# Kernel tuning notes

Measured on AMD Instinct MI355X. Metric: run time of the kernel, lower is better.

## Reference

```python
import jax, jax.numpy as jnp
import numpy as np

N_NODES = 100000
N_EDGES = 50000
NNZ = 1600000
D_IN = 128
D_OUT = 128  # heads(8) * out_channels(16)


def setup_inputs() -> dict:
    key = jax.random.key(0)
    k1, k2, k3, k4 = jax.random.split(key, 4)
    X = jax.random.normal(k1, (N_NODES, D_IN), dtype=jnp.float32)
    W = jax.random.normal(k2, (D_IN, D_OUT), dtype=jnp.float32) * (1.0 / np.sqrt(D_IN))
    eps = jnp.zeros((1,), dtype=jnp.float32)
    vertex = jax.random.randint(k3, (NNZ,), 0, N_NODES, dtype=jnp.int32)
    edges = jax.random.randint(k4, (NNZ,), 0, N_EDGES, dtype=jnp.int32)
    return {"X": X, "W": W, "eps": eps, "vertex": vertex, "edges": edges,
            "num_edges": N_EDGES}


def reference(X, W, eps, vertex, edges, num_edges):
    N = X.shape[0]
    Xp = X @ W                                   # [N, D_OUT] linear proj (no bias)
    Xve = Xp[vertex]                             # [nnz, D_OUT] vertex -> incidence gather
    Xe = jax.ops.segment_sum(Xve, edges, num_segments=num_edges)   # [E, D_OUT] first_aggregate='sum'
    Xev = Xe[edges]                              # [nnz, D_OUT] edge -> incidence gather
    Xv = jax.ops.segment_sum(Xev, vertex, num_segments=N)          # [N, D_OUT]
    out = (1.0 + eps) * Xp + Xv                  # GIN combine with learnable eps (eps is [1], broadcasts)
    return jax.nn.gelu(out, approximate=False)   # torch F.gelu default = exact erf
```

## Files before the change

kernel.cpp:

```cpp
#include <hip/hip_runtime.h>
#include <math.h>

#define NN 100000
#define NE 50000
#define NSEG (NE + NN)
#define DD 128

#define NBE 196
#define NBV 391
#define NB  (NBE + NBV)
#define CAP_E 8960
#define CAP_V 4608

typedef short bf16x8 __attribute__((ext_vector_type(8)));
typedef float f32x4 __attribute__((ext_vector_type(4)));
typedef float v2f __attribute__((ext_vector_type(2)));

static __device__ __forceinline__ float gelu_exact(float x) {
  return 0.5f * x * (1.0f + erff(x * 0.70710678118654752f));
}

static __device__ __forceinline__ int bucket_base(int g) {
  return (g < NBE) ? g * CAP_E : NBE * CAP_E + (g - NBE) * CAP_V;
}

static __device__ __forceinline__ void acc2(v2f& a, unsigned u) {
  union { unsigned i; float f; } lo, hi;
  lo.i = u << 16;
  hi.i = u & 0xFFFF0000u;
  v2f t;
  t.x = lo.f;
  t.y = hi.f;
  a += t;
}

static __device__ __forceinline__ void acc4(v2f* a, uint4 u) {
  acc2(a[0], u.x); acc2(a[1], u.y); acc2(a[2], u.z); acc2(a[3], u.w);
}

static __device__ __forceinline__ unsigned pack_bf16x2(float a, float b) {
  unsigned ua = __float_as_uint(a), ub = __float_as_uint(b);
  ua = (ua + 0x7FFFu + ((ua >> 16) & 1u)) >> 16;
  ub = (ub + 0x7FFFu + ((ub >> 16) & 1u)) >> 16;
  return ua | (ub << 16);
}

static __device__ __forceinline__ unsigned short bf16_rne(float a) {
  unsigned ua = __float_as_uint(a);
  ua = (ua + 0x7FFFu + ((ua >> 16) & 1u)) >> 16;
  return (unsigned short)ua;
}

static __device__ __forceinline__ void reduce8(v2f* a) {
#pragma unroll
  for (int k = 0; k < 4; ++k) {
    float x = a[k].x, y = a[k].y;
    x += __shfl_xor(x, 8);  y += __shfl_xor(y, 8);
    x += __shfl_xor(x, 16); y += __shfl_xor(y, 16);
    x += __shfl_xor(x, 32); y += __shfl_xor(y, 32);
    a[k].x = x; a[k].y = y;
  }
}

__global__ __launch_bounds__(256) void k_init(int* __restrict__ gcur,
                                              const float* __restrict__ W,
                                              unsigned short* __restrict__ Wt) {
  const int b = blockIdx.x;
  if (b < 64) {
    int idx = b * 256 + threadIdx.x;
    int k = idx >> 7, n = idx & 127;
    Wt[n * 128 + k] = bf16_rne(W[idx]);
  } else {
    int g = (b - 64) * 256 + threadIdx.x;
    if (g < NB) gcur[g] = bucket_base(g);
  }
}

__global__ __launch_bounds__(256) void k_gemm(const float* __restrict__ X,
                                              const unsigned short* __restrict__ Wt,
                                              unsigned short* __restrict__ Xb2h) {
  const int tid = threadIdx.x;
  const int w = tid >> 6;
  const int l = tid & 63;
  const int lm = l & 15;
  const int lk = l >> 4;
  const int R = blockIdx.x * 64 + w * 16;
  const int arow = R + lm;
  const bool rowok = arow < NN;
  const f32x4* __restrict__ X4 = (const f32x4*)X;
  const uint4* __restrict__ Wt4 = (const uint4*)Wt;

  f32x4 acc[8];
#pragma unroll
  for (int t = 0; t < 8; ++t) acc[t] = (f32x4)(0.f);

  for (int c = 0; c < 4; ++c) {
    const int k0 = c * 32 + lk * 8;
    f32x4 x0 = (f32x4)(0.f), x1 = (f32x4)(0.f);
    if (rowok) {
      x0 = __builtin_nontemporal_load(&X4[arow * 32 + (k0 >> 2)]);
      x1 = __builtin_nontemporal_load(&X4[arow * 32 + (k0 >> 2) + 1]);
    }
    union { bf16x8 v; uint4 u; } a;
    a.u.x = pack_bf16x2(x0.x, x0.y);
    a.u.y = pack_bf16x2(x0.z, x0.w);
    a.u.z = pack_bf16x2(x1.x, x1.y);
    a.u.w = pack_bf16x2(x1.z, x1.w);
#pragma unroll
    for (int t = 0; t < 8; ++t) {
      union { bf16x8 v; uint4 u; } b;
      b.u = Wt4[(t * 16 + lm) * 16 + c * 4 + lk];
      acc[t] = __builtin_amdgcn_mfma_f32_16x16x32_bf16(a.v, b.v, acc[t], 0, 0, 0);
    }
  }

  const int drow = R + lk * 4;
#pragma unroll
  for (int r = 0; r < 4; ++r) {
    const int row = drow + r;
    if (row < NN) {
#pragma unroll
      for (int t = 0; t < 8; ++t) {
        __builtin_nontemporal_store(
            bf16_rne(acc[t][r]),
            &Xb2h[((size_t)(t >> 2) * NN + row) * 64 + (t & 3) * 16 + lm]);
      }
    }
  }
}

__global__ __launch_bounds__(256) void k_pass1(const int* __restrict__ vertex,
                                               const int* __restrict__ edges,
                                               int* __restrict__ gcur,
                                               int* __restrict__ S, int nnz) {
  __shared__ int hist[NB];
  const int tid = threadIdx.x;
  for (int b = tid; b < NB; b += 256) hist[b] = 0;
  __syncthreads();
  const int base = blockIdx.x * 4096;
#pragma unroll
  for (int k = 0; k < 16; ++k) {
    int i = base + tid + k * 256;
    if (i < nnz) {
      atomicAdd(&hist[edges[i] >> 8], 1);
      atomicAdd(&hist[NBE + (vertex[i] >> 8)], 1);
    }
  }
  __syncthreads();
  for (int b = tid; b < NB; b += 256) {
    int c = hist[b];
    hist[b] = c ? atomicAdd(&gcur[b], c) : 0;
  }
  __syncthreads();
#pragma unroll
  for (int k = 0; k < 16; ++k) {
    int i = base + tid + k * 256;
    if (i < nnz) {
      int e = edges[i], v = vertex[i];
      int pe = atomicAdd(&hist[e >> 8], 1);
      S[pe] = ((e & 255) << 17) | v;
      int pv = atomicAdd(&hist[NBE + (v >> 8)], 1);
      S[pv] = ((v & 255) << 17) | e;
    }
  }
}

__global__ __launch_bounds__(256) void k_pass2(const int* __restrict__ gcur,
                                               const int* __restrict__ S,
                                               int* __restrict__ LE,
                                               unsigned short* __restrict__ LV,
                                               int* __restrict__ O, int nnz) {
  __shared__ int offs[257];
  __shared__ int cur[256];
  __shared__ int scratch[CAP_E];
  const int g = blockIdx.x;
  const int tid = threadIdx.x;
  int part = 0;
  for (int i = tid; i < g; i += 256) part += gcur[i] - bucket_base(i);
  cur[tid] = part;
  __syncthreads();
#pragma unroll
  for (int s2 = 128; s2 > 0; s2 >>= 1) {
    if (tid < s2) cur[tid] += cur[tid + s2];
    __syncthreads();
  }
  const bool isE = g < NBE;
  const int dbase = isE ? cur[0] : cur[0] - nnz;
  __syncthreads();

  const int sstart = bucket_base(g);
  int nit = gcur[g] - sstart;
  const int cap = isE ? CAP_E : CAP_V;
  if (nit > cap) nit = cap;
  const int s0 = isE ? (g << 8) : ((g - NBE) << 8);
  const int segN = min(256, (isE ? NE : NN) - s0);
  const int obase = isE ? s0 : NE + 1 + s0;
  for (int k = tid; k < 257; k += 256) offs[k] = 0;
  __syncthreads();
  for (int t = tid; t < nit; t += 256) atomicAdd(&offs[(S[sstart + t] >> 17) + 1], 1);
  __syncthreads();
  for (int off = 1; off < 256; off <<= 1) {
    int y = (tid >= off) ? offs[tid + 1 - off] : 0;
    __syncthreads();
    offs[tid + 1] += y;
    __syncthreads();
  }
  cur[tid] = offs[tid];
  __syncthreads();
  for (int t = tid; t < nit; t += 256) {
    int u = S[sstart + t];
    int r = atomicAdd(&cur[u >> 17], 1);
    scratch[r] = u & 0x1FFFF;
  }
  __syncthreads();
  if (isE) {
    for (int t = tid; t < nit; t += 256) LE[dbase + t] = scratch[t];
  } else {
    for (int t = tid; t < nit; t += 256) LV[dbase + t] = (unsigned short)scratch[t];
  }
  for (int k = tid; k <= segN; k += 256) O[obase + k] = dbase + offs[k];
}

__global__ __launch_bounds__(256) void k_edge_agg(const unsigned* __restrict__ Xb2h,
                                                  const int* __restrict__ O,
                                                  const int* __restrict__ LE,
                                                  unsigned* __restrict__ Xe2h) {
  const int h = blockIdx.y;
  const int e = blockIdx.x * 4 + (threadIdx.x >> 6);
  const int lane = threadIdx.x & 63;
  const int s = lane >> 3;
  const int r = lane & 7;
  const int start = O[e];
  const int end = O[e + 1];
  const uint4* __restrict__ P = (const uint4*)(Xb2h + (size_t)h * NN * 32);
  v2f a[4];
#pragma unroll
  for (int k = 0; k < 4; ++k) a[k] = (v2f)(0.f);
  int j = start + s;
  for (; j + 24 < end; j += 32) {
    int i0 = __builtin_nontemporal_load(&LE[j]);
    int i1 = __builtin_nontemporal_load(&LE[j + 8]);
    int i2 = __builtin_nontemporal_load(&LE[j + 16]);
    int i3 = __builtin_nontemporal_load(&LE[j + 24]);
    uint4 u0 = P[(size_t)i0 * 8 + r];
    uint4 u1 = P[(size_t)i1 * 8 + r];
    uint4 u2 = P[(size_t)i2 * 8 + r];
    uint4 u3 = P[(size_t)i3 * 8 + r];
    acc4(a, u0); acc4(a, u1); acc4(a, u2); acc4(a, u3);
  }
  if (j + 8 < end) {
    int i0 = __builtin_nontemporal_load(&LE[j]);
    int i1 = __builtin_nontemporal_load(&LE[j + 8]);
    uint4 u0 = P[(size_t)i0 * 8 + r];
    uint4 u1 = P[(size_t)i1 * 8 + r];
    acc4(a, u0); acc4(a, u1);
    j += 16;
  }
  if (j < end) {
    int i0 = __builtin_nontemporal_load(&LE[j]);
    acc4(a, P[(size_t)i0 * 8 + r]);
  }
  reduce8(a);
  const int p = s & 3;
  v2f sel = (p == 0) ? a[0] : (p == 1) ? a[1] : (p == 2) ? a[2] : a[3];
  unsigned pk = pack_bf16x2(sel.x, sel.y);
  if (s < 4) {
    __builtin_nontemporal_store(pk, &Xe2h[((size_t)h * NE + e) * 32 + r * 4 + p]);
  }
}

__global__ __launch_bounds__(256) void k_vert_agg(const unsigned* __restrict__ Xe2h,
                                                  const int* __restrict__ O,
                                                  const unsigned short* __restrict__ LV,
                                                  const float* __restrict__ eps,
                                                  const unsigned* __restrict__ Xb2h,
                                                  float* __restrict__ out) {
  const int h = blockIdx.y;
  const int v = blockIdx.x * 4 + (threadIdx.x >> 6);
  const int lane = threadIdx.x & 63;
  const int s = lane >> 3;
  const int r = lane & 7;
  const int start = O[NE + 1 + v];
  const int end = O[NE + 2 + v];
  const uint4* __restrict__ Q = (const uint4*)(Xe2h + (size_t)h * NE * 32);
  v2f a[4];
#pragma unroll
  for (int k = 0; k < 4; ++k) a[k] = (v2f)(0.f);
  int j = start + s;
  for (; j + 8 < end; j += 16) {
    int i0 = (int)__builtin_nontemporal_load(&LV[j]);
    int i1 = (int)__builtin_nontemporal_load(&LV[j + 8]);
    uint4 u0 = Q[(size_t)i0 * 8 + r];
    uint4 u1 = Q[(size_t)i1 * 8 + r];
    acc4(a, u0); acc4(a, u1);
  }
  if (j < end) {
    int i0 = (int)__builtin_nontemporal_load(&LV[j]);
    acc4(a, Q[(size_t)i0 * 8 + r]);
  }
  reduce8(a);
  const int p = s & 3;
  v2f sel = (p == 0) ? a[0] : (p == 1) ? a[1] : (p == 2) ? a[2] : a[3];
  unsigned su = __builtin_nontemporal_load(&Xb2h[((size_t)h * NN + v) * 32 + r * 4 + p]);
  union { unsigned i; float f; } plo, phi;
  plo.i = su << 16;
  phi.i = su & 0xFFFF0000u;
  const float sc = 1.0f + eps[0];
  v2f x;
  x.x = gelu_exact(fmaf(sc, plo.f, sel.x));
  x.y = gelu_exact(fmaf(sc, phi.f, sel.y));
  if (s < 4) {
    v2f* __restrict__ P2 = (v2f*)out;
    __builtin_nontemporal_store(x, &P2[(size_t)v * 64 + h * 32 + r * 4 + p]);
  }
}

extern "C" void kernel_launch(void* const* d_in, const int* in_sizes, int n_in,
                              void* d_out, int out_size, void* d_ws, size_t ws_size,
                              hipStream_t stream) {
  const float* X = (const float*)d_in[0];
  const float* W = (const float*)d_in[1];
  const float* eps = (const float*)d_in[2];
  const int* vertex = (const int*)d_in[3];
  const int* edges = (const int*)d_in[4];
  const int nnz = in_sizes[3];

  char* ws = (char*)d_ws;
  size_t off = 0;
  auto alloc = [&](size_t bytes) -> void* {
    void* p = ws + off;
    off = (off + bytes + 255) & ~(size_t)255;
    return p;
  };
  const size_t stagingB = ((size_t)NBE * CAP_E + (size_t)NBV * CAP_V) * 4;
  const size_t xbB = (size_t)NN * DD * 2;
  void* A = alloc(xbB > stagingB ? xbB : stagingB);
  int* S = (int*)A;
  unsigned short* Xb2h = (unsigned short*)A;
  unsigned* Xe2h = (unsigned*)alloc((size_t)NE * DD * 2);
  int* LE = (int*)alloc((size_t)nnz * sizeof(int));
  unsigned short* LV =
      (unsigned short*)alloc((size_t)nnz * sizeof(unsigned short));
  int* O = (int*)alloc((size_t)(NSEG + 2) * sizeof(int));
  int* gcur = (int*)alloc((size_t)NB * sizeof(int));
  unsigned short* Wt = (unsigned short*)alloc((size_t)DD * DD * 2);
  if (off > ws_size) return;

  k_init<<<67, 256, 0, stream>>>(gcur, W, Wt);
  k_pass1<<<(nnz + 4095) / 4096, 256, 0, stream>>>(vertex, edges, gcur, S, nnz);
  k_pass2<<<NB, 256, 0, stream>>>(gcur, S, LE, LV, O, nnz);
  k_gemm<<<(NN + 63) / 64, 256, 0, stream>>>(X, Wt, Xb2h);
  k_edge_agg<<<dim3(NE / 4, 2), 256, 0, stream>>>((const unsigned*)Xb2h, O, LE, Xe2h);
  k_vert_agg<<<dim3(NN / 4, 2), 256, 0, stream>>>(Xe2h, O, LV, eps,
                                                  (const unsigned*)Xb2h, (float*)d_out);
}
```

Baseline: 347.6 us.

## Drop head-split layout and gather full 256-byte rows per segment

Changes the bf16 projected and edge-feature buffers from a two-half, head-split layout to contiguous 128-wide rows. Each aggregation kernel now covers all 128 channels per segment in one pass, with 16 lanes per row and 4 rows in flight per wavefront. This halves the grid, reads each segment's index list once instead of twice, and shortens the cross-lane reduction. The trade is fewer independent rows per wave for short segments, and the GEMM stores lose their nontemporal hint.

```diff
diff --git a/kernel.cpp b/kernel.cpp
--- a/kernel.cpp
+++ b/kernel.cpp
@@ -51,11 +51,10 @@
   return (unsigned short)ua;
 }
 
-static __device__ __forceinline__ void reduce8(v2f* a) {
+static __device__ __forceinline__ void reduce4(v2f* a) {
 #pragma unroll
   for (int k = 0; k < 4; ++k) {
     float x = a[k].x, y = a[k].y;
-    x += __shfl_xor(x, 8);  y += __shfl_xor(y, 8);
     x += __shfl_xor(x, 16); y += __shfl_xor(y, 16);
     x += __shfl_xor(x, 32); y += __shfl_xor(y, 32);
     a[k].x = x; a[k].y = y;
@@ -78,7 +77,7 @@
 
 __global__ __launch_bounds__(256) void k_gemm(const float* __restrict__ X,
                                               const unsigned short* __restrict__ Wt,
-                                              unsigned short* __restrict__ Xb2h) {
+                                              unsigned short* __restrict__ Xb2) {
   const int tid = threadIdx.x;
   const int w = tid >> 6;
   const int l = tid & 63;
@@ -121,9 +120,7 @@
     if (row < NN) {
 #pragma unroll
       for (int t = 0; t < 8; ++t) {
-        __builtin_nontemporal_store(
-            bf16_rne(acc[t][r]),
-            &Xb2h[((size_t)(t >> 2) * NN + row) * 64 + (t & 3) * 16 + lm]);
+        Xb2[row * 128 + t * 16 + lm] = bf16_rne(acc[t][r]);
       }
     }
   }
@@ -221,87 +218,112 @@
   for (int k = tid; k <= segN; k += 256) O[obase + k] = dbase + offs[k];
 }
 
-__global__ __launch_bounds__(256) void k_edge_agg(const unsigned* __restrict__ Xb2h,
+__global__ __launch_bounds__(256) void k_edge_agg(const unsigned* __restrict__ Xb2,
                                                   const int* __restrict__ O,
                                                   const int* __restrict__ LE,
-                                                  unsigned* __restrict__ Xe2h) {
-  const int h = blockIdx.y;
+                                                  unsigned* __restrict__ Xe2) {
   const int e = blockIdx.x * 4 + (threadIdx.x >> 6);
   const int lane = threadIdx.x & 63;
-  const int s = lane >> 3;
-  const int r = lane & 7;
+  const int q = lane >> 4;
+  const int ql = lane & 15;
   const int start = O[e];
   const int end = O[e + 1];
-  const uint4* __restrict__ P = (const uint4*)(Xb2h + (size_t)h * NN * 32);
+  const uint4* __restrict__ P = (const uint4*)Xb2;
   v2f a[4];
 #pragma unroll
   for (int k = 0; k < 4; ++k) a[k] = (v2f)(0.f);
-  int j = start + s;
-  for (; j + 24 < end; j += 32) {
+  int j = start + q;
+  for (; j + 28 < end; j += 32) {
     int i0 = __builtin_nontemporal_load(&LE[j]);
-    int i1 = __builtin_nontemporal_load(&LE[j + 8]);
-    int i2 = __builtin_nontemporal_load(&LE[j + 16]);
-    int i3 = __builtin_nontemporal_load(&LE[j + 24]);
-    uint4 u0 = P[(size_t)i0 * 8 + r];
-    uint4 u1 = P[(size_t)i1 * 8 + r];
-    uint4 u2 = P[(size_t)i2 * 8 + r];
-    uint4 u3 = P[(size_t)i3 * 8 + r];
+    int i1 = __builtin_nontemporal_load(&LE[j + 4]);
+    int i2 = __builtin_nontemporal_load(&LE[j + 8]);
+    int i3 = __builtin_nontemporal_load(&LE[j + 12]);
+    int i4 = __builtin_nontemporal_load(&LE[j + 16]);
+    int i5 = __builtin_nontemporal_load(&LE[j + 20]);
+    int i6 = __builtin_nontemporal_load(&LE[j + 24]);
+    int i7 = __builtin_nontemporal_load(&LE[j + 28]);
+    uint4 u0 = P[(size_t)i0 * 16 + ql];
+    uint4 u1 = P[(size_t)i1 * 16 + ql];
+    uint4 u2 = P[(size_t)i2 * 16 + ql];
+    uint4 u3 = P[(size_t)i3 * 16 + ql];
+    uint4 u4 = P[(size_t)i4 * 16 + ql];
+    uint4 u5 = P[(size_t)i5 * 16 + ql];
+    uint4 u6 = P[(size_t)i6 * 16 + ql];
+    uint4 u7 = P[(size_t)i7 * 16 + ql];
     acc4(a, u0); acc4(a, u1); acc4(a, u2); acc4(a, u3);
-  }
-  if (j + 8 < end) {
+    acc4(a, u4); acc4(a, u5); acc4(a, u6); acc4(a, u7);
+  }
+  for (; j + 12 < end; j += 16) {
     int i0 = __builtin_nontemporal_load(&LE[j]);
-    int i1 = __builtin_nontemporal_load(&LE[j + 8]);
-    uint4 u0 = P[(size_t)i0 * 8 + r];
-    uint4 u1 = P[(size_t)i1 * 8 + r];
+    int i1 = __builtin_nontemporal_load(&LE[j + 4]);
+    int i2 = __builtin_nontemporal_load(&LE[j + 8]);
+    int i3 = __builtin_nontemporal_load(&LE[j + 12]);
+    uint4 u0 = P[(size_t)i0 * 16 + ql];
+    uint4 u1 = P[(size_t)i1 * 16 + ql];
+    uint4 u2 = P[(size_t)i2 * 16 + ql];
+    uint4 u3 = P[(size_t)i3 * 16 + ql];
+    acc4(a, u0); acc4(a, u1); acc4(a, u2); acc4(a, u3);
+  }
+  if (j + 4 < end) {
+    int i0 = __builtin_nontemporal_load(&LE[j]);
+    int i1 = __builtin_nontemporal_load(&LE[j + 4]);
+    uint4 u0 = P[(size_t)i0 * 16 + ql];
+    uint4 u1 = P[(size_t)i1 * 16 + ql];
     acc4(a, u0); acc4(a, u1);
-    j += 16;
+    j += 8;
   }
   if (j < end) {
     int i0 = __builtin_nontemporal_load(&LE[j]);
-    acc4(a, P[(size_t)i0 * 8 + r]);
-  }
-  reduce8(a);
-  const int p = s & 3;
-  v2f sel = (p == 0) ? a[0] : (p == 1) ? a[1] : (p == 2) ? a[2] : a[3];
-  unsigned pk = pack_bf16x2(sel.x, sel.y);
-  if (s < 4) {
-    __builtin_nontemporal_store(pk, &Xe2h[((size_t)h * NE + e) * 32 + r * 4 + p]);
-  }
-}
-
-__global__ __launch_bounds__(256) void k_vert_agg(const unsigned* __restrict__ Xe2h,
+    acc4(a, P[(size_t)i0 * 16 + ql]);
+  }
+  reduce4(a);
+  v2f sel = (q == 0) ? a[0] : (q == 1) ? a[1] : (q == 2) ? a[2] : a[3];
+  Xe2[e * 64 + ql * 4 + q] = pack_bf16x2(sel.x, sel.y);
+}
+
+__global__ __launch_bounds__(256) void k_vert_agg(const unsigned* __restrict__ Xe2,
                                                   const int* __restrict__ O,
                                                   const unsigned short* __restrict__ LV,
                                                   const float* __restrict__ eps,
-                                                  const unsigned* __restrict__ Xb2h,
+                                                  const unsigned* __restrict__ Xb2,
                                                   float* __restrict__ out) {
-  const int h = blockIdx.y;
   const int v = blockIdx.x * 4 + (threadIdx.x >> 6);
   const int lane = threadIdx.x & 63;
-  const int s = lane >> 3;
-  const int r = lane & 7;
+  const int q = lane >> 4;
+  const int ql = lane & 15;
   const int start = O[NE + 1 + v];
   const int end = O[NE + 2 + v];
-  const uint4* __restrict__ Q = (const uint4*)(Xe2h + (size_t)h * NE * 32);
+  const uint4* __restrict__ Q = (const uint4*)Xe2;
   v2f a[4];
 #pragma unroll
   for (int k = 0; k < 4; ++k) a[k] = (v2f)(0.f);
-  int j = start + s;
-  for (; j + 8 < end; j += 16) {
+  int j = start + q;
+  for (; j + 12 < end; j += 16) {
     int i0 = (int)__builtin_nontemporal_load(&LV[j]);
-    int i1 = (int)__builtin_nontemporal_load(&LV[j + 8]);
-    uint4 u0 = Q[(size_t)i0 * 8 + r];
-    uint4 u1 = Q[(size_t)i1 * 8 + r];
+    int i1 = (int)__builtin_nontemporal_load(&LV[j + 4]);
+    int i2 = (int)__builtin_nontemporal_load(&LV[j + 8]);
+    int i3 = (int)__builtin_nontemporal_load(&LV[j + 12]);
+    uint4 u0 = Q[(size_t)i0 * 16 + ql];
+    uint4 u1 = Q[(size_t)i1 * 16 + ql];
+    uint4 u2 = Q[(size_t)i2 * 16 + ql];
+    uint4 u3 = Q[(size_t)i3 * 16 + ql];
+    acc4(a, u0); acc4(a, u1); acc4(a, u2); acc4(a, u3);
+  }
+  if (j + 4 < end) {
+    int i0 = (int)__builtin_nontemporal_load(&LV[j]);
+    int i1 = (int)__builtin_nontemporal_load(&LV[j + 4]);
+    uint4 u0 = Q[(size_t)i0 * 16 + ql];
+    uint4 u1 = Q[(size_t)i1 * 16 + ql];
     acc4(a, u0); acc4(a, u1);
+    j += 8;
   }
   if (j < end) {
     int i0 = (int)__builtin_nontemporal_load(&LV[j]);
-    acc4(a, Q[(size_t)i0 * 8 + r]);
-  }
-  reduce8(a);
-  const int p = s & 3;
-  v2f sel = (p == 0) ? a[0] : (p == 1) ? a[1] : (p == 2) ? a[2] : a[3];
-  unsigned su = __builtin_nontemporal_load(&Xb2h[((size_t)h * NN + v) * 32 + r * 4 + p]);
+    acc4(a, Q[(size_t)i0 * 16 + ql]);
+  }
+  reduce4(a);
+  v2f sel = (q == 0) ? a[0] : (q == 1) ? a[1] : (q == 2) ? a[2] : a[3];
+  unsigned su = __builtin_nontemporal_load(&Xb2[v * 64 + ql * 4 + q]);
   union { unsigned i; float f; } plo, phi;
   plo.i = su << 16;
   phi.i = su & 0xFFFF0000u;
@@ -309,10 +331,8 @@
   v2f x;
   x.x = gelu_exact(fmaf(sc, plo.f, sel.x));
   x.y = gelu_exact(fmaf(sc, phi.f, sel.y));
-  if (s < 4) {
-    v2f* __restrict__ P2 = (v2f*)out;
-    __builtin_nontemporal_store(x, &P2[(size_t)v * 64 + h * 32 + r * 4 + p]);
-  }
+  v2f* __restrict__ P2 = (v2f*)out;
+  __builtin_nontemporal_store(x, &P2[(size_t)v * 64 + ql * 4 + q]);
 }
 
 extern "C" void kernel_launch(void* const* d_in, const int* in_sizes, int n_in,
@@ -336,8 +356,8 @@
   const size_t xbB = (size_t)NN * DD * 2;
   void* A = alloc(xbB > stagingB ? xbB : stagingB);
   int* S = (int*)A;
-  unsigned short* Xb2h = (unsigned short*)A;
-  unsigned* Xe2h = (unsigned*)alloc((size_t)NE * DD * 2);
+  unsigned short* Xb2 = (unsigned short*)A;
+  unsigned* Xe2 = (unsigned*)alloc((size_t)NE * DD * 2);
   int* LE = (int*)alloc((size_t)nnz * sizeof(int));
   unsigned short* LV =
       (unsigned short*)alloc((size_t)nnz * sizeof(unsigned short));
@@ -349,8 +369,8 @@
   k_init<<<67, 256, 0, stream>>>(gcur, W, Wt);
   k_pass1<<<(nnz + 4095) / 4096, 256, 0, stream>>>(vertex, edges, gcur, S, nnz);
   k_pass2<<<NB, 256, 0, stream>>>(gcur, S, LE, LV, O, nnz);
-  k_gemm<<<(NN + 63) / 64, 256, 0, stream>>>(X, Wt, Xb2h);
-  k_edge_agg<<<dim3(NE / 4, 2), 256, 0, stream>>>((const unsigned*)Xb2h, O, LE, Xe2h);
-  k_vert_agg<<<dim3(NN / 4, 2), 256, 0, stream>>>(Xe2h, O, LV, eps,
-                                                  (const unsigned*)Xb2h, (float*)d_out);
-}
+  k_gemm<<<(NN + 63) / 64, 256, 0, stream>>>(X, Wt, Xb2);
+  k_edge_agg<<<NE / 4, 256, 0, stream>>>((const unsigned*)Xb2, O, LE, Xe2);
+  k_vert_agg<<<NN / 4, 256, 0, stream>>>(Xe2, O, LV, eps, (const unsigned*)Xb2,
+                                         (float*)d_out);
+}
```

Result: faster. 314.9 us (-9.4%).
